# Kernel optimization log

Measured on AMD Instinct MI355X. Metric: run time of the kernel, lower is better.

The kernel has to match this reference:

```python
import jax, jax.numpy as jnp
import numpy as np

HIDDEN = 512
NHEADS = 8
ALPHA = 0.1
NUM_HOP = 4
MASK_VAL = -16384.0
LN_EPS = 1e-5


def setup_inputs() -> dict:
    key = jax.random.key(0)
    ks = jax.random.split(key, 10)
    B, N, H = 8, 1024, HIDDEN
    s = 1.0 / np.sqrt(H)
    x = jax.random.normal(ks[0], (B, N, H), dtype=jnp.float32)
    adj = jax.random.randint(ks[1], (B, N, N), 0, 2, dtype=jnp.int32)
    Wq = jax.random.uniform(ks[2], (H, H), jnp.float32, -s, s)
    bq = jax.random.uniform(ks[3], (H,), jnp.float32, -s, s)
    Wk = jax.random.uniform(ks[4], (H, H), jnp.float32, -s, s)
    bk = jax.random.uniform(ks[5], (H,), jnp.float32, -s, s)
    Wv = jax.random.uniform(ks[6], (H, H), jnp.float32, -s, s)
    bv = jax.random.uniform(ks[7], (H,), jnp.float32, -s, s)
    gamma = jnp.ones((H,), jnp.float32)
    beta = jnp.zeros((H,), jnp.float32)
    return {"x": x, "adj": adj, "Wq": Wq, "bq": bq, "Wk": Wk, "bk": bk,
            "Wv": Wv, "bv": bv, "gamma": gamma, "beta": beta}


def reference(x, adj, Wq, bq, Wk, bk, Wv, bv, gamma, beta):
    B, N, H = x.shape
    u = H // NHEADS
    # torch Linear: y = x @ W^T + b
    q = x @ Wq.T + bq  # [B,N,H]
    k = x @ Wk.T + bk
    v = x @ Wv.T + bv
    # split hidden into contiguous head chunks (matches per-head slicing)
    qh = q.reshape(B, N, NHEADS, u).transpose(0, 2, 1, 3)  # [B,Hd,N,u]
    kh = k.reshape(B, N, NHEADS, u).transpose(0, 2, 1, 3)
    vh = v.reshape(B, N, NHEADS, u).transpose(0, 2, 1, 3)
    scores = jnp.einsum('bhnd,bhmd->bhnm', qh, kh)  # [B,Hd,N,N]
    mask = (adj == 0)[:, None, :, :]  # broadcast over heads
    scores = jnp.where(mask, MASK_VAL, scores)
    pros = jax.nn.softmax(scores, axis=-1)
    z_init = vh
    z = z_init
    for _ in range(NUM_HOP):
        z = (1.0 - ALPHA) * jnp.einsum('bhnm,bhmd->bhnd', pros, z) + ALPHA * z_init
    h_prime = z.transpose(0, 2, 1, 3).reshape(B, N, H)  # concat heads
    y = x + h_prime
    mu = jnp.mean(y, axis=-1, keepdims=True)
    var = jnp.mean((y - mu) ** 2, axis=-1, keepdims=True)
    return (y - mu) / jnp.sqrt(var + LN_EPS) * gamma + beta
```

## Files before the change

### kernel.cpp

```cpp
#include <hip/hip_runtime.h>
#include <hip/hip_bf16.h>

#define BB 8
#define NN 1024
#define HH 512
#define NHEADS 8
#define UU 64
#define MASK_VAL -16384.0f

typedef __attribute__((ext_vector_type(8))) short short8;
typedef __attribute__((ext_vector_type(4))) float f32x4;
typedef unsigned short u16;
typedef unsigned char u8;

__device__ inline float b2f(unsigned short u) {
    union { float f; unsigned int i; } c; c.i = ((unsigned int)u) << 16; return c.f;
}
__device__ inline unsigned short f2b(float f) {
    __hip_bfloat16 h = __float2bfloat16(f);
    return *reinterpret_cast<unsigned short*>(&h);
}
__device__ inline void gl_lds16(const void* g, void* l) {
    __builtin_amdgcn_global_load_lds(
        (const __attribute__((address_space(1))) unsigned int*)g,
        (__attribute__((address_space(3))) unsigned int*)l, 16, 0, 0);
}
__device__ inline u8 f2fp8(float f) {
    return (u8)__builtin_amdgcn_cvt_pk_fp8_f32(f, f, 0, false);
}

__global__ __launch_bounds__(256) void cvt_bf16(
    const float* __restrict__ x, const float* __restrict__ Wq,
    const float* __restrict__ Wk, const float* __restrict__ Wv,
    u16* __restrict__ xb, u16* __restrict__ Wb)
{
    const int which = blockIdx.y;
    const float* src;
    u16* dst;
    int n;
    if (which == 0) { src = x;  dst = xb;              n = BB * NN * HH; }
    else if (which == 1) { src = Wq; dst = Wb;             n = HH * HH; }
    else if (which == 2) { src = Wk; dst = Wb + HH * HH;   n = HH * HH; }
    else              { src = Wv; dst = Wb + 2 * HH * HH;  n = HH * HH; }

    const int base = (blockIdx.x * 256 + threadIdx.x) * 8;
    if (base >= n) return;
    const float4* sp = (const float4*)&src[base];
    float4 a = sp[0], b = sp[1];
    short8 o;
    o[0] = (short)f2b(a.x); o[1] = (short)f2b(a.y);
    o[2] = (short)f2b(a.z); o[3] = (short)f2b(a.w);
    o[4] = (short)f2b(b.x); o[5] = (short)f2b(b.y);
    o[6] = (short)f2b(b.z); o[7] = (short)f2b(b.w);
    *(short8*)&dst[base] = o;
}

__global__ __launch_bounds__(256) void qkv_gemm(
    const u16* __restrict__ xb, const u16* __restrict__ Wb,
    const float* __restrict__ bq, const float* __restrict__ bk,
    const float* __restrict__ bv,
    u16* __restrict__ q, u16* __restrict__ k, u16* __restrict__ v)
{
    const int which = blockIdx.z;
    const u16* W      = Wb + which * HH * HH;
    const float* bias = which == 0 ? bq : (which == 1 ? bk : bv);
    u16* out          = which == 0 ? q  : (which == 1 ? k  : v);

    const int tid = threadIdx.x;
    const int wave = tid >> 6, lane = tid & 63;
    const int ln = lane & 15, quad = lane >> 4;
    const int wr = (wave >> 1) * 64, wc = (wave & 1) * 64;
    const int rowbase = blockIdx.x * 128, colbase = blockIdx.y * 128;

    __shared__ __align__(16) u16 As[128 * 32];
    __shared__ __align__(16) u16 Bs[128 * 32];

    f32x4 acc[4][4];
    #pragma unroll
    for (int ri = 0; ri < 4; ++ri)
        #pragma unroll
        for (int ci = 0; ci < 4; ++ci) acc[ri][ci] = (f32x4){0.f, 0.f, 0.f, 0.f};

    const int lr = lane >> 2;
    const int lk = (lane & 3) * 8;

    for (int kk = 0; kk < HH; kk += 32) {
        __syncthreads();
        #pragma unroll
        for (int i = 0; i < 2; ++i) {
            int r = wave * 32 + i * 16 + lr;
            gl_lds16(&xb[(size_t)(rowbase + r) * HH + kk + lk],
                     (char*)As + (wave * 32 + i * 16) * 64);
            gl_lds16(&W[(size_t)(colbase + r) * HH + kk + lk],
                     (char*)Bs + (wave * 32 + i * 16) * 64);
        }
        __syncthreads();

        short8 bfr[4];
        #pragma unroll
        for (int ci = 0; ci < 4; ++ci)
            bfr[ci] = *(const short8*)&Bs[(wc + ci * 16 + ln) * 32 + quad * 8];
        #pragma unroll
        for (int ri = 0; ri < 4; ++ri) {
            short8 af = *(const short8*)&As[(wr + ri * 16 + ln) * 32 + quad * 8];
            #pragma unroll
            for (int ci = 0; ci < 4; ++ci)
                acc[ri][ci] = __builtin_amdgcn_mfma_f32_16x16x32_bf16(af, bfr[ci], acc[ri][ci], 0, 0, 0);
        }
    }

    #pragma unroll
    for (int ci = 0; ci < 4; ++ci) {
        int col = colbase + wc + ci * 16 + ln;
        int hh = col >> 6, dd = col & 63;
        float bb = bias[col];
        #pragma unroll
        for (int ri = 0; ri < 4; ++ri) {
            #pragma unroll
            for (int r = 0; r < 4; ++r) {
                int row = rowbase + wr + ri * 16 + quad * 4 + r;
                int bidx = row >> 10, n = row & 1023;
                out[(((size_t)(bidx * NHEADS + hh)) * NN + n) * UU + dd] = f2b(acc[ri][ci][r] + bb);
            }
        }
    }
}

__global__ __launch_bounds__(256) void scores_softmax(
    const u16* __restrict__ q, const u16* __restrict__ kmat,
    const int* __restrict__ adj, u8* __restrict__ P8)
{
    const int b = blockIdx.z, h = blockIdx.y, rt = blockIdx.x;
    const int bh = b * NHEADS + h;
    const int wave = threadIdx.x >> 6, lane = threadIdx.x & 63;
    const int ln = lane & 15, quad = lane >> 4;
    const int rowbase = rt * 16;

    __shared__ float redsum[4][16];

    const u16* qp = &q[((size_t)bh * NN + rowbase + ln) * UU + quad * 8];
    short8 a0 = *(const short8*)qp;
    short8 a1 = *(const short8*)(qp + 32);

    f32x4 accs[16];
    #pragma unroll
    for (int ct = 0; ct < 16; ++ct) {
        int col = wave * 256 + ct * 16 + ln;
        const u16* kp = &kmat[((size_t)bh * NN + col) * UU + quad * 8];
        short8 b0 = *(const short8*)kp;
        short8 b1 = *(const short8*)(kp + 32);
        f32x4 acc = (f32x4){0.f, 0.f, 0.f, 0.f};
        acc = __builtin_amdgcn_mfma_f32_16x16x32_bf16(a0, b0, acc, 0, 0, 0);
        acc = __builtin_amdgcn_mfma_f32_16x16x32_bf16(a1, b1, acc, 0, 0, 0);
        accs[ct] = acc;
    }

    float rsum[4] = {0.f, 0.f, 0.f, 0.f};
    #pragma unroll
    for (int ct = 0; ct < 16; ++ct) {
        int col = wave * 256 + ct * 16 + ln;
        #pragma unroll
        for (int r = 0; r < 4; ++r) {
            int row = rowbase + quad * 4 + r;
            float e = adj[((size_t)(b * NN + row)) * NN + col]
                        ? __expf(accs[ct][r] - 32.0f) : 0.0f;
            accs[ct][r] = e;
            rsum[r] += e;
        }
    }
    #pragma unroll
    for (int r = 0; r < 4; ++r) {
        #pragma unroll
        for (int off = 8; off >= 1; off >>= 1)
            rsum[r] += __shfl_xor(rsum[r], off);
    }
    if (ln == 0) {
        #pragma unroll
        for (int r = 0; r < 4; ++r) redsum[wave][quad * 4 + r] = rsum[r];
    }
    __syncthreads();
    float sc16[4];
    #pragma unroll
    for (int r = 0; r < 4; ++r) {
        int row16 = quad * 4 + r;
        float s = redsum[0][row16] + redsum[1][row16] + redsum[2][row16] + redsum[3][row16];
        sc16[r] = 16.0f / s;
    }

    u8* Pb = P8 + ((size_t)bh << 20) + rt * 16384;
    #pragma unroll
    for (int ct = 0; ct < 16; ++ct) {
        int kc = wave * 8 + (ct >> 1);
        int cb = (ct & 1) * 16 + ln;
        #pragma unroll
        for (int r = 0; r < 4; ++r)
            Pb[kc * 512 + (quad * 4 + r) * 32 + cb] = f2fp8(accs[ct][r] * sc16[r]);
    }
}

__global__ __launch_bounds__(256) void vt8(
    const u16* __restrict__ v, u8* __restrict__ v8t)
{
    const int bh = blockIdx.x;
    const int t = threadIdx.x;
    const size_t hd = (size_t)bh << 16;
    __shared__ u16 tile[64][72];

    for (int chunk = 0; chunk < 16; ++chunk) {
        const int n0 = chunk * 64;
        const int r = t >> 2, cs = t & 3;
        const u16* vp = &v[((size_t)bh * NN + n0 + r) * UU + cs * 16];
        short8 a = *(const short8*)vp;
        short8 b8 = *(const short8*)(vp + 8);
        #pragma unroll
        for (int j = 0; j < 8; ++j) {
            tile[r][cs * 16 + j] = (u16)a[j];
            tile[r][cs * 16 + 8 + j] = (u16)b8[j];
        }
        __syncthreads();
        const int c = t & 63, qt = t >> 6;
        unsigned int w[4];
        #pragma unroll
        for (int g = 0; g < 4; ++g) {
            float f0 = b2f(tile[qt * 16 + g * 4 + 0][c]);
            float f1 = b2f(tile[qt * 16 + g * 4 + 1][c]);
            float f2 = b2f(tile[qt * 16 + g * 4 + 2][c]);
            float f3 = b2f(tile[qt * 16 + g * 4 + 3][c]);
            int lo = __builtin_amdgcn_cvt_pk_fp8_f32(f0, f1, 0, false);
            w[g] = (unsigned int)__builtin_amdgcn_cvt_pk_fp8_f32(f2, f3, lo, true);
        }
        uint4 o; o.x = w[0]; o.y = w[1]; o.z = w[2]; o.w = w[3];
        *(uint4*)&v8t[hd + (size_t)c * 1024 + n0 + qt * 16] = o;
        __syncthreads();
    }
}

__global__ __launch_bounds__(512) void hop(
    const u8* __restrict__ P8, const u8* __restrict__ z8in,
    const u16* __restrict__ v, u8* __restrict__ z8out,
    u16* __restrict__ zbf_out, int last)
{
    const int b = blockIdx.z, h = blockIdx.y, rt = blockIdx.x;
    const int bh = b * NHEADS + h;
    const int tid = threadIdx.x;
    const int wave = tid >> 6, lane = tid & 63;
    const int ln = lane & 15, quad = lane >> 4;
    const int wrow = rt * 128 + wave * 16;

    __shared__ __align__(16) u8 zt[64 * 1040];

    const u8* zg = z8in + ((size_t)bh << 16);
    #pragma unroll
    for (int i = 0; i < 8; ++i) {
        int c = wave * 8 + i;
        gl_lds16(zg + (size_t)c * 1024 + lane * 16, (char*)zt + c * 1040);
    }
    __syncthreads();

    f32x4 acc[4];
    #pragma unroll
    for (int ci = 0; ci < 4; ++ci) acc[ci] = (f32x4){0.f, 0.f, 0.f, 0.f};

    const u8* pt = P8 + ((size_t)bh << 20) + (size_t)(rt * 8 + wave) * 16384
                 + ln * 32 + quad * 8;
    #pragma unroll 4
    for (int kc = 0; kc < 32; ++kc) {
        long a = *(const long*)(pt + kc * 512);
        int kk = kc * 32;
        #pragma unroll
        for (int ci = 0; ci < 4; ++ci) {
            long bz = *(const long*)&zt[(ci * 16 + ln) * 1040 + kk + quad * 8];
            acc[ci] = __builtin_amdgcn_mfma_f32_16x16x32_fp8_fp8(a, bz, acc[ci], 0, 0, 0);
        }
    }

    if (last) {
        #pragma unroll
        for (int ci = 0; ci < 4; ++ci) {
            int col = ci * 16 + ln;
            #pragma unroll
            for (int r = 0; r < 4; ++r) {
                int row = wrow + quad * 4 + r;
                float vv = b2f(v[((size_t)bh * NN + row) * UU + col]);
                zbf_out[((size_t)(b * NN + row)) * HH + h * UU + col]
                    = f2b(0.05625f * acc[ci][r] + 0.1f * vv);
            }
        }
    } else {
        u8* zo = z8out + ((size_t)bh << 16);
        #pragma unroll
        for (int ci = 0; ci < 4; ++ci) {
            int col = ci * 16 + ln;
            float zv[4];
            #pragma unroll
            for (int r = 0; r < 4; ++r) {
                int row = wrow + quad * 4 + r;
                float vv = b2f(v[((size_t)bh * NN + row) * UU + col]);
                zv[r] = 0.05625f * acc[ci][r] + 0.1f * vv;
            }
            int lo = __builtin_amdgcn_cvt_pk_fp8_f32(zv[0], zv[1], 0, false);
            unsigned int dw = (unsigned int)__builtin_amdgcn_cvt_pk_fp8_f32(zv[2], zv[3], lo, true);
            *(unsigned int*)&zo[(size_t)col * 1024 + wrow + quad * 4] = dw;
        }
    }
}

__global__ __launch_bounds__(256) void resid_ln(
    const float* __restrict__ x, const u16* __restrict__ z,
    const float* __restrict__ gamma, const float* __restrict__ beta,
    float* __restrict__ out)
{
    const int r = blockIdx.x * 4 + (threadIdx.x >> 6);
    const int lane = threadIdx.x & 63;
    const size_t base = (size_t)r * HH + lane * 8;

    const float4* xp = (const float4*)&x[base];
    float4 x0 = xp[0], x1 = xp[1];
    short8 zv = *(const short8*)&z[base];
    float y[8];
    y[0] = x0.x + b2f((u16)zv[0]); y[1] = x0.y + b2f((u16)zv[1]);
    y[2] = x0.z + b2f((u16)zv[2]); y[3] = x0.w + b2f((u16)zv[3]);
    y[4] = x1.x + b2f((u16)zv[4]); y[5] = x1.y + b2f((u16)zv[5]);
    y[6] = x1.z + b2f((u16)zv[6]); y[7] = x1.w + b2f((u16)zv[7]);

    float s = 0.f, sq = 0.f;
    #pragma unroll
    for (int j = 0; j < 8; ++j) { s += y[j]; sq += y[j] * y[j]; }
    #pragma unroll
    for (int off = 32; off >= 1; off >>= 1) {
        s  += __shfl_xor(s, off);
        sq += __shfl_xor(sq, off);
    }
    const float mu = s * (1.0f / HH);
    const float var = sq * (1.0f / HH) - mu * mu;
    const float rstd = rsqrtf(var + 1e-5f);

    const float4* gp = (const float4*)&gamma[lane * 8];
    const float4* bp = (const float4*)&beta[lane * 8];
    float4 g0 = gp[0], g1 = gp[1], b0 = bp[0], b1 = bp[1];

    float4 o0, o1;
    o0.x = (y[0] - mu) * rstd * g0.x + b0.x;
    o0.y = (y[1] - mu) * rstd * g0.y + b0.y;
    o0.z = (y[2] - mu) * rstd * g0.z + b0.z;
    o0.w = (y[3] - mu) * rstd * g0.w + b0.w;
    o1.x = (y[4] - mu) * rstd * g1.x + b1.x;
    o1.y = (y[5] - mu) * rstd * g1.y + b1.y;
    o1.z = (y[6] - mu) * rstd * g1.z + b1.z;
    o1.w = (y[7] - mu) * rstd * g1.w + b1.w;
    float4* op = (float4*)&out[base];
    op[0] = o0; op[1] = o1;
}

extern "C" void kernel_launch(void* const* d_in, const int* in_sizes, int n_in,
                              void* d_out, int out_size, void* d_ws, size_t ws_size,
                              hipStream_t stream)
{
    const float* x   = (const float*)d_in[0];
    const int* adj   = (const int*)d_in[1];
    const float* Wq  = (const float*)d_in[2];
    const float* bq  = (const float*)d_in[3];
    const float* Wk  = (const float*)d_in[4];
    const float* bk  = (const float*)d_in[5];
    const float* Wv  = (const float*)d_in[6];
    const float* bv  = (const float*)d_in[7];
    const float* gamma = (const float*)d_in[8];
    const float* beta  = (const float*)d_in[9];
    float* out = (float*)d_out;

    const size_t E = (size_t)BB * NN * HH;
    u16* ws16 = (u16*)d_ws;
    u16* xb = ws16;
    u16* q  = ws16 + E;
    u16* k  = ws16 + 2 * E;
    u16* v  = ws16 + 3 * E;
    u16* za = ws16 + 4 * E;
    u16* Wb = ws16 + 5 * E;
    u8* base8 = (u8*)(ws16 + 5 * E + 786432);
    u8* P8  = base8;
    u8* z8a = base8 + ((size_t)64 << 20);
    u8* z8b = z8a + ((size_t)4 << 20);
    u8* v8t = z8b + ((size_t)4 << 20);

    cvt_bf16<<<dim3(2048, 4), 256, 0, stream>>>(x, Wq, Wk, Wv, xb, Wb);
    qkv_gemm<<<dim3(64, 4, 3), 256, 0, stream>>>(xb, Wb, bq, bk, bv, q, k, v);
    scores_softmax<<<dim3(64, NHEADS, BB), 256, 0, stream>>>(q, k, adj, P8);
    vt8<<<dim3(64), 256, 0, stream>>>(v, v8t);
    hop<<<dim3(8, NHEADS, BB), 512, 0, stream>>>(P8, v8t, v, z8a, za, 0);
    hop<<<dim3(8, NHEADS, BB), 512, 0, stream>>>(P8, z8a, v, z8b, za, 0);
    hop<<<dim3(8, NHEADS, BB), 512, 0, stream>>>(P8, z8b, v, z8a, za, 0);
    hop<<<dim3(8, NHEADS, BB), 512, 0, stream>>>(P8, z8a, v, z8b, za, 1);
    resid_ln<<<dim3(2048), 256, 0, stream>>>(x, za, gamma, beta, out);
}
```

Baseline: 300.4 us.

## Bit-pack adjacency once and stage softmax fp8 output through LDS

```diff
diff --git a/kernel.cpp b/kernel.cpp
--- a/kernel.cpp
+++ b/kernel.cpp
@@ -6,7 +6,6 @@
 #define HH 512
 #define NHEADS 8
 #define UU 64
-#define MASK_VAL -16384.0f
 
 typedef __attribute__((ext_vector_type(8))) short short8;
 typedef __attribute__((ext_vector_type(4))) float f32x4;
@@ -55,6 +54,21 @@
     *(short8*)&dst[base] = o;
 }
 
+__global__ __launch_bounds__(256) void adj_pack(
+    const int* __restrict__ adj, unsigned int* __restrict__ adjp)
+{
+    const int wave = threadIdx.x >> 6, lane = threadIdx.x & 63;
+    const int row = blockIdx.x * 4 + wave;
+    const int* ar = adj + (size_t)row * NN;
+    unsigned long long* out = (unsigned long long*)(adjp + (size_t)row * 32);
+    #pragma unroll
+    for (int it = 0; it < 16; ++it) {
+        int a = ar[it * 64 + lane];
+        unsigned long long m = __ballot(a != 0);
+        if (lane == 0) out[it] = m;
+    }
+}
+
 __global__ __launch_bounds__(256) void qkv_gemm(
     const u16* __restrict__ xb, const u16* __restrict__ Wb,
     const float* __restrict__ bq, const float* __restrict__ bk,
@@ -128,7 +142,7 @@
 
 __global__ __launch_bounds__(256) void scores_softmax(
     const u16* __restrict__ q, const u16* __restrict__ kmat,
-    const int* __restrict__ adj, u8* __restrict__ P8)
+    const unsigned int* __restrict__ adjp, u8* __restrict__ P8)
 {
     const int b = blockIdx.z, h = blockIdx.y, rt = blockIdx.x;
     const int bh = b * NHEADS + h;
@@ -137,10 +151,20 @@
     const int rowbase = rt * 16;
 
     __shared__ float redsum[4][16];
+    __shared__ __align__(16) u8 Pst[16384];
 
     const u16* qp = &q[((size_t)bh * NN + rowbase + ln) * UU + quad * 8];
     short8 a0 = *(const short8*)qp;
     short8 a1 = *(const short8*)(qp + 32);
+
+    unsigned int abits[4][8];
+    #pragma unroll
+    for (int r = 0; r < 4; ++r) {
+        int row = rowbase + quad * 4 + r;
+        const uint4* ap = (const uint4*)&adjp[((size_t)(b * NN + row)) * 32 + wave * 8];
+        *(uint4*)&abits[r][0] = ap[0];
+        *(uint4*)&abits[r][4] = ap[1];
+    }
 
     f32x4 accs[16];
     #pragma unroll
@@ -158,12 +182,12 @@
     float rsum[4] = {0.f, 0.f, 0.f, 0.f};
     #pragma unroll
     for (int ct = 0; ct < 16; ++ct) {
-        int col = wave * 256 + ct * 16 + ln;
+        const int kc8 = ct >> 1;
+        const int bitpos = (ct & 1) * 16 + ln;
         #pragma unroll
         for (int r = 0; r < 4; ++r) {
-            int row = rowbase + quad * 4 + r;
-            float e = adj[((size_t)(b * NN + row)) * NN + col]
-                        ? __expf(accs[ct][r] - 32.0f) : 0.0f;
+            unsigned int on = (abits[r][kc8] >> bitpos) & 1u;
+            float e = on ? __expf(accs[ct][r] - 32.0f) : 0.0f;
             accs[ct][r] = e;
             rsum[r] += e;
         }
@@ -187,15 +211,20 @@
         sc16[r] = 16.0f / s;
     }
 
-    u8* Pb = P8 + ((size_t)bh << 20) + rt * 16384;
     #pragma unroll
     for (int ct = 0; ct < 16; ++ct) {
         int kc = wave * 8 + (ct >> 1);
         int cb = (ct & 1) * 16 + ln;
         #pragma unroll
         for (int r = 0; r < 4; ++r)
-            Pb[kc * 512 + (quad * 4 + r) * 32 + cb] = f2fp8(accs[ct][r] * sc16[r]);
-    }
+            Pst[kc * 512 + (quad * 4 + r) * 32 + cb] = f2fp8(accs[ct][r] * sc16[r]);
+    }
+    __syncthreads();
+
+    u8* Pb = P8 + ((size_t)bh << 20) + rt * 16384;
+    const uint4* srcp = (const uint4*)(Pst + threadIdx.x * 64);
+    uint4* dstp = (uint4*)(Pb + threadIdx.x * 64);
+    dstp[0] = srcp[0]; dstp[1] = srcp[1]; dstp[2] = srcp[2]; dstp[3] = srcp[3];
 }
 
 __global__ __launch_bounds__(256) void vt8(
@@ -381,10 +410,12 @@
     u8* z8a = base8 + ((size_t)64 << 20);
     u8* z8b = z8a + ((size_t)4 << 20);
     u8* v8t = z8b + ((size_t)4 << 20);
+    unsigned int* adjp = (unsigned int*)(v8t + ((size_t)4 << 20));
 
     cvt_bf16<<<dim3(2048, 4), 256, 0, stream>>>(x, Wq, Wk, Wv, xb, Wb);
+    adj_pack<<<dim3(2048), 256, 0, stream>>>(adj, adjp);
     qkv_gemm<<<dim3(64, 4, 3), 256, 0, stream>>>(xb, Wb, bq, bk, bv, q, k, v);
-    scores_softmax<<<dim3(64, NHEADS, BB), 256, 0, stream>>>(q, k, adj, P8);
+    scores_softmax<<<dim3(64, NHEADS, BB), 256, 0, stream>>>(q, k, adjp, P8);
     vt8<<<dim3(64), 256, 0, stream>>>(v, v8t);
     hop<<<dim3(8, NHEADS, BB), 512, 0, stream>>>(P8, v8t, v, z8a, za, 0);
     hop<<<dim3(8, NHEADS, BB), 512, 0, stream>>>(P8, z8a, v, z8b, za, 0);
```

Result: no change. 304.9 us (+1.5%).
